# Kernel optimization log

Measured on AMD Instinct MI355X. Metric: run time of the kernel, lower is better.

Reference implementation:

```python
import jax, jax.numpy as jnp
import numpy as np

B, R, H, W = 128, 8, 256, 256


def _conv(x, w, b):
    # x: [1, C_in, h, w], w: [C_out, C_in, 3, 3]; stride 2, pad 1, then bias + ReLU
    y = jax.lax.conv_general_dilated(
        x, w, window_strides=(2, 2), padding=((1, 1), (1, 1)),
        dimension_numbers=('NCHW', 'OIHW', 'NCHW'))
    return jax.nn.relu(y + b[None, :, None, None])


def _single(x, w1, b1, w2, b2, w3, b3, fw, fb):
    # x: [3, H, W]; one sample through its region's CNN expert
    h = x[None]                      # [1,3,H,W]
    h = _conv(h, w1, b1)             # [1,32,H/2,W/2]
    h = _conv(h, w2, b2)             # [1,64,H/4,W/4]
    h = _conv(h, w3, b3)             # [1,128,H/8,W/8]
    feat = h.mean(axis=(2, 3))[0]    # [128] global average pool
    return fw @ feat + fb            # [num_classes]


def setup_inputs() -> dict:
    key = jax.random.key(0)
    ks = jax.random.split(key, 10)
    s = 0.05
    return {
        'image': jax.random.normal(ks[0], (B, 3, H, W), jnp.float32),
        'region': jax.random.randint(ks[1], (B,), 0, R, jnp.int64),
        'w1': jax.random.normal(ks[2], (R, 32, 3, 3, 3), jnp.float32) * s,
        'b1': jax.random.normal(ks[3], (R, 32), jnp.float32) * s,
        'w2': jax.random.normal(ks[4], (R, 64, 32, 3, 3), jnp.float32) * s,
        'b2': jax.random.normal(ks[5], (R, 64), jnp.float32) * s,
        'w3': jax.random.normal(ks[6], (R, 128, 64, 3, 3), jnp.float32) * s,
        'b3': jax.random.normal(ks[7], (R, 128), jnp.float32) * s,
        'fw': jax.random.normal(ks[8], (R, 2, 128), jnp.float32) * s,
        'fb': jax.random.normal(ks[9], (R, 2), jnp.float32) * s,
    }


def reference(image, region, w1, b1, w2, b2, w3, b3, fw, fb):
    # MoE-style dispatch: gather each sample's region weights, vmap per-sample expert.
    r = region.astype(jnp.int32)
    pw = [jnp.take(p, r, axis=0) for p in (w1, b1, w2, b2, w3, b3, fw, fb)]
    out = jax.vmap(_single)(image, *pw)  # [B, num_classes]
    return out
```

## Files before the change

### kernel.cpp

```cpp
#include <hip/hip_runtime.h>
#include <cstdint>


typedef __attribute__((ext_vector_type(8))) short short8;
typedef __attribute__((ext_vector_type(4))) float floatx4;
typedef __attribute__((ext_vector_type(4))) unsigned short ushort4v;
typedef __attribute__((ext_vector_type(4))) float float4v;

__device__ inline unsigned short f2bf(float f) {
  union { float f; unsigned u; } x;
  x.f = f;
  unsigned u = x.u;
  u += 0x7FFFu + ((u >> 16) & 1u);
  return (unsigned short)(u >> 16);
}

__device__ inline void g2l16(const unsigned short* g, unsigned short* l) {
  __builtin_amdgcn_global_load_lds(
      (const __attribute__((address_space(1))) unsigned int*)g,
      (__attribute__((address_space(3))) unsigned int*)(unsigned int)(uintptr_t)l,
      16, 0, 0);
}

__global__ __launch_bounds__(128) void prep_k(const int* __restrict__ rp,
                                              int* __restrict__ rout,
                                              float* __restrict__ feat) {
  __shared__ int is64;
  if (threadIdx.x == 0) {
    int odd_or = 0;
    for (int i = 0; i < 64; ++i) odd_or |= rp[2 * i + 1];
    is64 = (odd_or == 0) ? 1 : 0;
  }
  __syncthreads();
  int b = threadIdx.x;
  int r = is64 ? rp[2 * b] : rp[b];
  rout[b] = r & 7;
  float* fr = feat + b * 128;
  for (int j = 0; j < 128; ++j) fr[j] = 0.f;
}

__global__ __launch_bounds__(256) void pack1_k(const float* __restrict__ w,
                                               unsigned short* __restrict__ dst) {
  int t = blockIdx.x * blockDim.x + threadIdx.x;
  if (t >= 16384) return;
  int j = t & 7, lane = (t >> 3) & 63, mt = (t >> 9) & 1, kg = (t >> 10) & 1,
      r = t >> 11;
  int oc = mt * 16 + (lane & 15);
  int q = (lane >> 4) & 3;
  int row = kg * 2 + (q >> 1);
  int idx = (q & 1) * 8 + j;
  int kx = idx >> 2, c = idx & 3;
  float val = 0.f;
  if (row < 3 && kx < 3 && c < 3) val = w[((r * 32 + oc) * 3 + c) * 9 + row * 3 + kx];
  dst[t] = f2bf(val);
}

template <int OC, int IC, int SUBK, int MTG>
__global__ __launch_bounds__(256) void packT_k(const float* __restrict__ w,
                                               unsigned short* __restrict__ dst) {
  const int total = 8 * 9 * SUBK * MTG * 512;
  int t = blockIdx.x * blockDim.x + threadIdx.x;
  if (t >= total) return;
  int j = t & 7, lane = (t >> 3) & 63;
  int u = t >> 9;
  int mt = u % MTG; u /= MTG;
  int s = u % SUBK; u /= SUBK;
  int tap = u % 9;
  int r = u / 9;
  int oc = mt * 16 + (lane & 15);
  int ic = s * 32 + ((lane >> 4) & 3) * 8 + j;
  dst[t] = f2bf(w[((r * OC + oc) * IC + ic) * 9 + tap]);
}

__global__ __launch_bounds__(256) void halo8_k(unsigned short* __restrict__ buf,
                                               int nplane, int HP, int WP) {
  int per = 2 * WP + 2 * (HP - 2);
  int t = blockIdx.x * blockDim.x + threadIdx.x;
  if (t >= nplane * per) return;
  int s = t / per, i = t - s * per;
  int y, x;
  if (i < WP) { y = 0; x = i; }
  else if (i < 2 * WP) { y = HP - 1; x = i - WP; }
  else {
    int ii = i - 2 * WP;
    y = 1 + (ii >> 1);
    x = (ii & 1) ? (WP - 1) : 0;
  }
  short8 z = {0, 0, 0, 0, 0, 0, 0, 0};
  *(short8*)(buf + ((size_t)s * HP * WP + y * WP + x) * 8) = z;
}

__global__ __launch_bounds__(256, 2) void conv12_k(
    const float* __restrict__ img, const unsigned short* __restrict__ w1p,
    const float* __restrict__ b1, const unsigned short* __restrict__ w2p,
    const float* __restrict__ b2, const int* __restrict__ rgn,
    unsigned short* __restrict__ outp, int b0) {
  __shared__ unsigned short imgT[19 * 168 * 4];
  __shared__ unsigned short h1T[9 * 4 * 66 * 8];
  __shared__ float sB1[32];
  __shared__ float sB2[64];
  const int tid = threadIdx.x;
  const int xh = blockIdx.x;
  const int oy0 = blockIdx.y * 4;
  const int bl = blockIdx.z;
  const int r = __builtin_amdgcn_readfirstlane(rgn[b0 + bl]);
  if (tid < 32) sB1[tid] = b1[r * 32 + tid];
  if (tid >= 64 && tid < 128) sB2[tid - 64] = b2[r * 64 + (tid - 64)];
  const float* ib = img + (size_t)(b0 + bl) * 3 * 65536;
  const int padx = xh ? 65 : 0;
  const bool skiptop = (oy0 == 0);

  const int rb = xh * 128 - 4;
  for (int seg = 0; seg < 779; seg += 256) {
    int c = seg + tid;
    if (c < 779) {
      int row = c / 41, cq = c - row * 41;
      int rv = 4 * oy0 - 3 + row;
      int cb = rb + 4 * cq;
      unsigned short* dp = &imgT[((size_t)row * 168 + (4 * cq - 1)) * 4];
      bool vr = (rv >= 0);
      if (vr && cq > 0 && cb >= 0 && cb + 3 <= 255) {
        const float* p = ib + (size_t)rv * 256 + cb;
        float4v a = *(const float4v*)p;
        float4v bb = *(const float4v*)(p + 65536);
        float4v cc = *(const float4v*)(p + 131072);
#pragma unroll
        for (int i = 0; i < 4; ++i) {
          ushort4v v = {f2bf(a[i]), f2bf(bb[i]), f2bf(cc[i]), 0};
          *(ushort4v*)(dp + i * 4) = v;
        }
      } else {
        for (int i = (cq == 0 ? 1 : 0); i < 4; ++i) {
          int cc2 = cb + i;
          ushort4v v = {0, 0, 0, 0};
          if (vr && cc2 >= 0 && cc2 <= 255) {
            const float* p = ib + (size_t)rv * 256 + cc2;
            v.x = f2bf(p[0]);
            v.y = f2bf(p[65536]);
            v.z = f2bf(p[131072]);
          }
          *(ushort4v*)(dp + i * 4) = v;
        }
      }
    }
  }
  {
    short8 z8 = {0, 0, 0, 0, 0, 0, 0, 0};
    if (tid < 36) {
      int hy = tid / 4, cg = tid % 4;
      *(short8*)&h1T[(((size_t)hy * 4 + cg) * 66 + padx) * 8] = z8;
    }
    if (skiptop) {
      for (int c = tid; c < 264; c += 256) {
        int cg = c / 66, x = c - cg * 66;
        *(short8*)&h1T[(((size_t)0 * 4 + cg) * 66 + x) * 8] = z8;
      }
    }
  }

  const int n = tid & 15, q = (tid >> 4) & 3, wv = tid >> 6;
  const int lane = tid & 63;
  const short8* wpb1 = (const short8*)w1p + (size_t)r * 256 + lane;
  short8 afr1[2][2];
#pragma unroll
  for (int kg = 0; kg < 2; ++kg)
#pragma unroll
    for (int m = 0; m < 2; ++m) afr1[kg][m] = wpb1[(kg * 2 + m) * 64];

  __syncthreads();

#pragma unroll
  for (int rep = 0; rep < 3; ++rep) {
    int hy = wv + 4 * rep;
    if (hy <= 8) {
      floatx4 a1[5][2];
#pragma unroll
      for (int nt = 0; nt < 5; ++nt)
#pragma unroll
        for (int m = 0; m < 2; ++m) a1[nt][m] = (floatx4){0.f, 0.f, 0.f, 0.f};
#pragma unroll
      for (int kg = 0; kg < 2; ++kg) {
        int row = kg * 2 + (q >> 1);
        int rowc = (row < 3) ? row : 0;
        int tr = 2 * hy + rowc;
#pragma unroll
        for (int nt = 0; nt < 5; ++nt) {
          int lx = nt * 16 + n;
          short8 bfr = *(const short8*)&imgT[((size_t)tr * 168 + 2 * lx) * 4 +
                                             (q & 1) * 8];
#pragma unroll
          for (int m = 0; m < 2; ++m)
            a1[nt][m] = __builtin_amdgcn_mfma_f32_16x16x32_bf16(
                afr1[kg][m], bfr, a1[nt][m], 0, 0, 0);
        }
      }
#pragma unroll
      for (int nt = 0; nt < 5; ++nt) {
        int lx = nt * 16 + n;
        bool ok = (lx <= 65) && (lx != padx) && !(skiptop && hy == 0);
        if (ok) {
#pragma unroll
          for (int m = 0; m < 2; ++m) {
            ushort4v st;
#pragma unroll
            for (int rr = 0; rr < 4; ++rr) {
              float v = a1[nt][m][rr] + sB1[m * 16 + q * 4 + rr];
              st[rr] = f2bf(v > 0.f ? v : 0.f);
            }
            int cg = m * 2 + (q >> 1);
            *(ushort4v*)&h1T[(((size_t)hy * 4 + cg) * 66 + lx) * 8 +
                             (q & 1) * 4] = st;
          }
        }
      }
    }
  }
  __syncthreads();

  const short8* wpb2 = (const short8*)w2p + (size_t)r * 9 * 4 * 64 + lane;
  floatx4 a2[2][4];
#pragma unroll
  for (int nt = 0; nt < 2; ++nt)
#pragma unroll
    for (int m = 0; m < 4; ++m) a2[nt][m] = (floatx4){0.f, 0.f, 0.f, 0.f};
#pragma unroll
  for (int tap = 0; tap < 9; ++tap) {
    const int ky = tap / 3, kx = tap % 3;
    short8 af[4];
#pragma unroll
    for (int m = 0; m < 4; ++m) af[m] = wpb2[(tap * 4 + m) * 64];
    short8 bf[2];
#pragma unroll
    for (int nt = 0; nt < 2; ++nt) {
      int ox = nt * 16 + n;
      bf[nt] = *(const short8*)&h1T[((((2 * wv + ky) << 2) + q) * 66 +
                                    (2 * ox + kx)) * 8];
    }
#pragma unroll
    for (int m = 0; m < 4; ++m)
#pragma unroll
      for (int nt = 0; nt < 2; ++nt)
        a2[nt][m] = __builtin_amdgcn_mfma_f32_16x16x32_bf16(af[m], bf[nt],
                                                            a2[nt][m], 0, 0, 0);
  }
  unsigned short* ob = outp + (size_t)bl * 8 * 66 * 66 * 8;
  const int oy = oy0 + wv;
#pragma unroll
  for (int nt = 0; nt < 2; ++nt) {
    int ox = xh * 32 + nt * 16 + n;
#pragma unroll
    for (int m = 0; m < 4; ++m) {
      ushort4v st;
#pragma unroll
      for (int rr = 0; rr < 4; ++rr) {
        float v = a2[nt][m][rr] + sB2[m * 16 + q * 4 + rr];
        st[rr] = f2bf(v > 0.f ? v : 0.f);
      }
      int cg = m * 2 + (q >> 1);
      *(ushort4v*)&ob[(((size_t)cg * 66 + oy + 1) * 66 + ox + 1) * 8 +
                      (q & 1) * 4] = st;
    }
  }
}

__global__ __launch_bounds__(128, 2) void conv3lds_k(
    const unsigned short* __restrict__ in, const unsigned short* __restrict__ wp,
    const float* __restrict__ bias, const int* __restrict__ rgn,
    float* __restrict__ feat, int b0) {
  __shared__ unsigned short tile[9 * 4 * 66 * 8];
  __shared__ float sBias[128];
  __shared__ float sGap[2 * 128];
  const int tid = threadIdx.x;
  const int bl = blockIdx.y;
  const int b = b0 + bl;
  const int r = __builtin_amdgcn_readfirstlane(rgn[b]);
  sBias[tid] = bias[r * 128 + tid];
  const int oy0 = blockIdx.x * 4;
  const unsigned short* gbase = in + (size_t)bl * 8 * 66 * 66 * 8;
  const int lane = tid & 63, wv = tid >> 6;
  const int n = lane & 15, q = (lane >> 4) & 3;
  const short8* wpb = (const short8*)wp + (size_t)r * 9 * 2 * 8 * 64 + lane;
  floatx4 acc[4][8];
#pragma unroll
  for (int nt = 0; nt < 4; ++nt)
#pragma unroll
    for (int m = 0; m < 8; ++m) acc[nt][m] = (floatx4){0.f, 0.f, 0.f, 0.f};
#pragma unroll
  for (int s = 0; s < 2; ++s) {
    __syncthreads();
    for (int seg = 0; seg < 2376; seg += 128) {
      int c = seg + tid;
      if (c < 2376) {
        int iy = c / 264;
        int rem = c - iy * 264;
        int c8 = rem / 66;
        int x = rem - c8 * 66;
        const unsigned short* gp =
            gbase + (((size_t)(s * 4 + c8) * 66 + 2 * oy0 + iy) * 66 + x) * 8;
        g2l16(gp, tile + (size_t)(seg + wv * 64) * 8);
      }
    }
    __syncthreads();
#pragma unroll
    for (int tap = 0; tap < 9; ++tap) {
      const int ky = tap / 3, kx = tap % 3;
      short8 afr[8];
#pragma unroll
      for (int m = 0; m < 8; ++m) afr[m] = wpb[((tap * 2 + s) * 8 + m) * 64];
      short8 bfr[4];
#pragma unroll
      for (int nt = 0; nt < 4; ++nt) {
        int oyl = 2 * wv + (nt >> 1);
        int ox = ((nt & 1) << 4) + n;
        bfr[nt] = *(const short8*)&tile[(((2 * oyl + ky) * 4 + q) * 66 +
                                        (2 * ox + kx)) * 8];
      }
#pragma unroll
      for (int m = 0; m < 8; ++m)
#pragma unroll
        for (int nt = 0; nt < 4; ++nt)
          acc[nt][m] = __builtin_amdgcn_mfma_f32_16x16x32_bf16(afr[m], bfr[nt],
                                                               acc[nt][m], 0, 0, 0);
    }
  }
#pragma unroll
  for (int m = 0; m < 8; ++m)
#pragma unroll
    for (int rr = 0; rr < 4; ++rr) {
      float bv = sBias[m * 16 + q * 4 + rr];
      float vs = 0.f;
#pragma unroll
      for (int nt = 0; nt < 4; ++nt) {
        float v = acc[nt][m][rr] + bv;
        vs += (v > 0.f ? v : 0.f);
      }
      vs += __shfl_xor(vs, 1, 16);
      vs += __shfl_xor(vs, 2, 16);
      vs += __shfl_xor(vs, 4, 16);
      vs += __shfl_xor(vs, 8, 16);
      if (n == 0) sGap[wv * 128 + m * 16 + q * 4 + rr] = vs;
    }
  __syncthreads();
  atomicAdd(&feat[b * 128 + tid], sGap[tid] + sGap[128 + tid]);
}

__global__ __launch_bounds__(256) void head_k(
    const float* __restrict__ feat, const float* __restrict__ fw,
    const float* __restrict__ fb, const int* __restrict__ rgn,
    float* __restrict__ out) {
  int t = threadIdx.x;
  int b = t >> 1, c = t & 1;
  int r = rgn[b];
  const float* fwr = fw + (r * 2 + c) * 128;
  const float* fv = feat + b * 128;
  float a = 0.f;
#pragma unroll 8
  for (int j = 0; j < 128; ++j) a = fmaf(fwr[j], fv[j], a);
  out[t] = a * (1.0f / 1024.0f) + fb[r * 2 + c];
}

extern "C" void kernel_launch(void* const* d_in, const int* in_sizes, int n_in,
                              void* d_out, int out_size, void* d_ws, size_t ws_size,
                              hipStream_t stream) {
  const float* img = (const float*)d_in[0];
  const int* rgn_raw = (const int*)d_in[1];
  const float* w1 = (const float*)d_in[2];
  const float* b1 = (const float*)d_in[3];
  const float* w2 = (const float*)d_in[4];
  const float* b2 = (const float*)d_in[5];
  const float* w3 = (const float*)d_in[6];
  const float* b3 = (const float*)d_in[7];
  const float* fw = (const float*)d_in[8];
  const float* fb = (const float*)d_in[9];
  float* out = (float*)d_out;

  const size_t h2p_s = (size_t)8 * 66 * 66 * 8 * 2;
  const size_t per_sample = h2p_s;
  const size_t fixed = (size_t)16384 * 2 + (size_t)147456 * 2 +
                       (size_t)589824 * 2 + 128 * 128 * 4 + 512 + 16 * 256;
  int C = 128;
  while (C > 1 && fixed + (size_t)C * per_sample > ws_size) C >>= 1;

  char* ws = (char*)d_ws;
  size_t off = 0;
  auto alloc = [&](size_t bytes) {
    char* p = ws + off;
    off += (bytes + 255) & ~(size_t)255;
    return p;
  };
  unsigned short* h2p = (unsigned short*)alloc((size_t)C * h2p_s);
  unsigned short* w1p = (unsigned short*)alloc((size_t)16384 * 2);
  unsigned short* w2p = (unsigned short*)alloc((size_t)147456 * 2);
  unsigned short* w3p = (unsigned short*)alloc((size_t)589824 * 2);
  float* feat = (float*)alloc((size_t)128 * 128 * 4);
  int* rgn = (int*)alloc((size_t)128 * 4);

  hipLaunchKernelGGL(prep_k, dim3(1), dim3(128), 0, stream, rgn_raw, rgn, feat);
  hipLaunchKernelGGL(pack1_k, dim3(64), dim3(256), 0, stream, w1, w1p);
  hipLaunchKernelGGL((packT_k<64, 32, 1, 4>), dim3(576), dim3(256), 0, stream, w2, w2p);
  hipLaunchKernelGGL((packT_k<128, 64, 2, 8>), dim3(2304), dim3(256), 0, stream, w3, w3p);
  {
    int n2 = C * 8 * (2 * 66 + 2 * 64);
    hipLaunchKernelGGL(halo8_k, dim3((n2 + 255) / 256), dim3(256), 0, stream,
                       h2p, C * 8, 66, 66);
  }

  for (int b0 = 0; b0 < 128; b0 += C) {
    hipLaunchKernelGGL(conv12_k, dim3(2, 16, C), dim3(256), 0, stream,
                       img, w1p, b1, w2p, b2, rgn, h2p, b0);
    hipLaunchKernelGGL(conv3lds_k, dim3(8, C), dim3(128), 0, stream,
                       h2p, w3p, b3, rgn, feat, b0);
  }
  hipLaunchKernelGGL(head_k, dim3(1), dim3(256), 0, stream, feat, fw, fb, rgn, out);
}
```

Measured before the change: 301.9 us.

## Stage conv1 input in two ring-buffer phases to cut LDS and raise occupancy

The fp32-to-bf16 image tile staged in LDS shrinks from 19 rows to an 11-row buffer. It is filled in two phases: rows 0-10 first, then rows 11-18 wrapped into the same slots. Conv1 output rows are split to match, so rows 0-4 read phase A and rows 5-8 read phase B. Less shared memory allows launch bounds to request 3 blocks per CU instead of 2, at the cost of two extra barriers and a serialized second staging pass in which no conv1 MFMA work overlaps.

```diff
diff --git a/kernel.cpp b/kernel.cpp
--- a/kernel.cpp
+++ b/kernel.cpp
@@ -90,12 +90,12 @@
   *(short8*)(buf + ((size_t)s * HP * WP + y * WP + x) * 8) = z;
 }
 
-__global__ __launch_bounds__(256, 2) void conv12_k(
+__global__ __launch_bounds__(256, 3) void conv12_k(
     const float* __restrict__ img, const unsigned short* __restrict__ w1p,
     const float* __restrict__ b1, const unsigned short* __restrict__ w2p,
     const float* __restrict__ b2, const int* __restrict__ rgn,
     unsigned short* __restrict__ outp, int b0) {
-  __shared__ unsigned short imgT[19 * 168 * 4];
+  __shared__ unsigned short imgT[11 * 168 * 4];
   __shared__ unsigned short h1T[9 * 4 * 66 * 8];
   __shared__ float sB1[32];
   __shared__ float sB2[64];
@@ -109,41 +109,98 @@
   const float* ib = img + (size_t)(b0 + bl) * 3 * 65536;
   const int padx = xh ? 65 : 0;
   const bool skiptop = (oy0 == 0);
-
   const int rb = xh * 128 - 4;
-  for (int seg = 0; seg < 779; seg += 256) {
-    int c = seg + tid;
-    if (c < 779) {
-      int row = c / 41, cq = c - row * 41;
-      int rv = 4 * oy0 - 3 + row;
-      int cb = rb + 4 * cq;
-      unsigned short* dp = &imgT[((size_t)row * 168 + (4 * cq - 1)) * 4];
-      bool vr = (rv >= 0);
-      if (vr && cq > 0 && cb >= 0 && cb + 3 <= 255) {
-        const float* p = ib + (size_t)rv * 256 + cb;
-        float4v a = *(const float4v*)p;
-        float4v bb = *(const float4v*)(p + 65536);
-        float4v cc = *(const float4v*)(p + 131072);
-#pragma unroll
-        for (int i = 0; i < 4; ++i) {
-          ushort4v v = {f2bf(a[i]), f2bf(bb[i]), f2bf(cc[i]), 0};
-          *(ushort4v*)(dp + i * 4) = v;
+
+  const int n = tid & 15, q = (tid >> 4) & 3, wv = tid >> 6;
+  const int lane = tid & 63;
+  const short8* wpb1 = (const short8*)w1p + (size_t)r * 256 + lane;
+  short8 afr1[2][2];
+#pragma unroll
+  for (int kg = 0; kg < 2; ++kg)
+#pragma unroll
+    for (int m = 0; m < 2; ++m) afr1[kg][m] = wpb1[(kg * 2 + m) * 64];
+
+  auto STAGE = [&](int t0, int nrows) {
+    const int nch = nrows * 41;
+    for (int seg = 0; seg < nch; seg += 256) {
+      int c = seg + tid;
+      if (c < nch) {
+        int i = c / 41, cq = c - i * 41;
+        int rv = 4 * oy0 - 3 + t0 + i;
+        int cb = rb + 4 * cq;
+        unsigned short* dp = &imgT[((size_t)i * 168 + (4 * cq - 1)) * 4];
+        if (rv >= 0 && cq > 0 && cb >= 0 && cb + 3 <= 255) {
+          const float* p = ib + (size_t)rv * 256 + cb;
+          float4v a = *(const float4v*)p;
+          float4v bb = *(const float4v*)(p + 65536);
+          float4v cc = *(const float4v*)(p + 131072);
+#pragma unroll
+          for (int e = 0; e < 4; ++e) {
+            ushort4v v = {f2bf(a[e]), f2bf(bb[e]), f2bf(cc[e]), 0};
+            *(ushort4v*)(dp + e * 4) = v;
+          }
+        } else {
+          for (int e = (cq == 0 ? 1 : 0); e < 4; ++e) {
+            int cc2 = cb + e;
+            ushort4v v = {0, 0, 0, 0};
+            if (rv >= 0 && cc2 >= 0 && cc2 <= 255) {
+              const float* p = ib + (size_t)rv * 256 + cc2;
+              v.x = f2bf(p[0]);
+              v.y = f2bf(p[65536]);
+              v.z = f2bf(p[131072]);
+            }
+            *(ushort4v*)(dp + e * 4) = v;
+          }
         }
-      } else {
-        for (int i = (cq == 0 ? 1 : 0); i < 4; ++i) {
-          int cc2 = cb + i;
-          ushort4v v = {0, 0, 0, 0};
-          if (vr && cc2 >= 0 && cc2 <= 255) {
-            const float* p = ib + (size_t)rv * 256 + cc2;
-            v.x = f2bf(p[0]);
-            v.y = f2bf(p[65536]);
-            v.z = f2bf(p[131072]);
+      }
+    }
+  };
+
+  auto CONV1ROW = [&](int hy, int phaseB) {
+    floatx4 a1[5][2];
+#pragma unroll
+    for (int nt = 0; nt < 5; ++nt)
+#pragma unroll
+      for (int m = 0; m < 2; ++m) a1[nt][m] = (floatx4){0.f, 0.f, 0.f, 0.f};
+#pragma unroll
+    for (int kg = 0; kg < 2; ++kg) {
+      int row = kg * 2 + (q >> 1);
+      int rowc = (row < 3) ? row : 0;
+      int tr = 2 * hy + rowc;
+      int slot = phaseB ? (tr >= 11 ? tr - 11 : tr) : tr;
+#pragma unroll
+      for (int nt = 0; nt < 5; ++nt) {
+        int lx = nt * 16 + n;
+        short8 bfr = *(const short8*)&imgT[((size_t)slot * 168 + 2 * lx) * 4 +
+                                           (q & 1) * 8];
+#pragma unroll
+        for (int m = 0; m < 2; ++m)
+          a1[nt][m] = __builtin_amdgcn_mfma_f32_16x16x32_bf16(
+              afr1[kg][m], bfr, a1[nt][m], 0, 0, 0);
+      }
+    }
+#pragma unroll
+    for (int nt = 0; nt < 5; ++nt) {
+      int lx = nt * 16 + n;
+      bool ok = (lx <= 65) && (lx != padx) && !(skiptop && hy == 0);
+      if (ok) {
+#pragma unroll
+        for (int m = 0; m < 2; ++m) {
+          ushort4v st;
+#pragma unroll
+          for (int rr = 0; rr < 4; ++rr) {
+            float v = a1[nt][m][rr] + sB1[m * 16 + q * 4 + rr];
+            st[rr] = f2bf(v > 0.f ? v : 0.f);
           }
-          *(ushort4v*)(dp + i * 4) = v;
+          int cg = m * 2 + (q >> 1);
+          *(ushort4v*)&h1T[(((size_t)hy * 4 + cg) * 66 + lx) * 8 +
+                           (q & 1) * 4] = st;
         }
       }
     }
-  }
+  };
+
+  STAGE(0, 11);
   {
     short8 z8 = {0, 0, 0, 0, 0, 0, 0, 0};
     if (tid < 36) {
@@ -157,64 +214,15 @@
       }
     }
   }
-
-  const int n = tid & 15, q = (tid >> 4) & 3, wv = tid >> 6;
-  const int lane = tid & 63;
-  const short8* wpb1 = (const short8*)w1p + (size_t)r * 256 + lane;
-  short8 afr1[2][2];
-#pragma unroll
-  for (int kg = 0; kg < 2; ++kg)
-#pragma unroll
-    for (int m = 0; m < 2; ++m) afr1[kg][m] = wpb1[(kg * 2 + m) * 64];
-
-  __syncthreads();
-
-#pragma unroll
-  for (int rep = 0; rep < 3; ++rep) {
-    int hy = wv + 4 * rep;
-    if (hy <= 8) {
-      floatx4 a1[5][2];
-#pragma unroll
-      for (int nt = 0; nt < 5; ++nt)
-#pragma unroll
-        for (int m = 0; m < 2; ++m) a1[nt][m] = (floatx4){0.f, 0.f, 0.f, 0.f};
-#pragma unroll
-      for (int kg = 0; kg < 2; ++kg) {
-        int row = kg * 2 + (q >> 1);
-        int rowc = (row < 3) ? row : 0;
-        int tr = 2 * hy + rowc;
-#pragma unroll
-        for (int nt = 0; nt < 5; ++nt) {
-          int lx = nt * 16 + n;
-          short8 bfr = *(const short8*)&imgT[((size_t)tr * 168 + 2 * lx) * 4 +
-                                             (q & 1) * 8];
-#pragma unroll
-          for (int m = 0; m < 2; ++m)
-            a1[nt][m] = __builtin_amdgcn_mfma_f32_16x16x32_bf16(
-                afr1[kg][m], bfr, a1[nt][m], 0, 0, 0);
-        }
-      }
-#pragma unroll
-      for (int nt = 0; nt < 5; ++nt) {
-        int lx = nt * 16 + n;
-        bool ok = (lx <= 65) && (lx != padx) && !(skiptop && hy == 0);
-        if (ok) {
-#pragma unroll
-          for (int m = 0; m < 2; ++m) {
-            ushort4v st;
-#pragma unroll
-            for (int rr = 0; rr < 4; ++rr) {
-              float v = a1[nt][m][rr] + sB1[m * 16 + q * 4 + rr];
-              st[rr] = f2bf(v > 0.f ? v : 0.f);
-            }
-            int cg = m * 2 + (q >> 1);
-            *(ushort4v*)&h1T[(((size_t)hy * 4 + cg) * 66 + lx) * 8 +
-                             (q & 1) * 4] = st;
-          }
-        }
-      }
-    }
-  }
+  __syncthreads();
+
+  for (int hy = wv; hy <= 4; hy += 4) CONV1ROW(hy, 0);
+  __syncthreads();
+
+  STAGE(11, 8);
+  __syncthreads();
+
+  CONV1ROW(5 + wv, 1);
   __syncthreads();
 
   const short8* wpb2 = (const short8*)w2p + (size_t)r * 9 * 4 * 64 + lane;
```

New measurement: 287.1 us. 4.9% less time.
